# Kernel optimization log

Hardware: AMD Instinct MI355X
Metric: run time of the kernel (lower is better)

The kernel has to match this reference:

```python
import jax, jax.numpy as jnp
import numpy as np

K = 4            # number of modes (init kwarg)
ALPHA = 2000.0   # bandwidth constraint
TAU = 0.0        # dual ascent step (0 -> exact reconstruction slack)
N_ITERS = 20     # fixed ADMM iterations (orig: tol-based while loop, max 500)


def vmd_batch(x):
    # x: [B, C, T] float32 -> (u: [B, C, K, T], omega: [B, C, K])
    B, C, T = x.shape
    T2 = 2 * T
    half = T2 // 2
    # mirror extension (vmdpy): flip first half | signal | flip second half
    f = jnp.concatenate([x[..., :T // 2][..., ::-1], x, x[..., T // 2:][..., ::-1]], axis=-1)  # [B,C,T2]
    t = jnp.arange(1, T2 + 1, dtype=jnp.float32) / T2
    freqs = t - 0.5 - 1.0 / T2                       # [T2], centered frequency axis
    freqs_pos = freqs[half:]                          # [T], positive frequencies
    f_hat = jnp.fft.fftshift(jnp.fft.fft(f, axis=-1), axes=-1).astype(jnp.complex64)
    f_hat_plus = f_hat.at[..., :half].set(0.0)        # keep analytic (positive-freq) part
    # init=1: uniform initial center frequencies
    omega = jnp.broadcast_to((0.5 / K) * jnp.arange(K, dtype=jnp.float32), (B, C, K))
    u_hat = jnp.zeros((B, C, K, T2), dtype=jnp.complex64)
    lam = jnp.zeros((B, C, T2), dtype=jnp.complex64)  # dual variable lambda_hat

    def step(carry, _):
        u_hat, omega, lam = carry
        S = jnp.sum(u_hat, axis=2)                    # running sum of all modes [B,C,T2]
        new_u, new_w = [], []
        for k in range(K):                            # Gauss-Seidel sweep over K modes (K small, unrolled)
            S = S - u_hat[:, :, k]                    # sum of all other modes (updated ones included)
            denom = 1.0 + ALPHA * (freqs[None, None, :] - omega[:, :, k:k + 1]) ** 2
            uk = (f_hat_plus - S + lam / 2.0) / denom # Wiener-filter spectral update [B,C,T2]
            S = S + uk
            p = uk.real[..., half:] ** 2 + uk.imag[..., half:] ** 2  # power on positive freqs [B,C,T]
            wk = jnp.sum(freqs_pos * p, axis=-1) / jnp.sum(p, axis=-1)  # center-frequency re-estimate
            new_u.append(uk)
            new_w.append(wk)
        u_hat = jnp.stack(new_u, axis=2)
        omega = jnp.stack(new_w, axis=-1)
        lam = lam + TAU * (S - f_hat_plus)            # dual ascent (tau=0 -> no-op, kept for fidelity)
        return (u_hat, omega, lam), None

    (u_hat, omega, lam), _ = jax.lax.scan(step, (u_hat, omega, lam), None, length=N_ITERS)

    # reconstruct full conjugate-symmetric spectrum
    pos = u_hat[..., half:]                           # [B,C,K,T]
    full = jnp.zeros((B, C, K, T2), dtype=jnp.complex64)
    full = full.at[..., half:].set(pos)
    full = full.at[..., 1:half + 1].set(jnp.conj(pos)[..., ::-1])  # full[half-j] = conj(pos[j])
    full = full.at[..., 0].set(jnp.conj(full[..., -1]))
    u = jnp.real(jnp.fft.ifft(jnp.fft.ifftshift(full, axes=-1), axis=-1))  # [B,C,K,T2]
    u = u[..., T2 // 4: 3 * T2 // 4]                  # de-mirror: center T samples
    return u, omega


def setup_inputs() -> dict:
    key = jax.random.key(0)
    x = jax.random.normal(key, (16, 8192, 4), dtype=jnp.float32)  # [B, T, C]
    return {"x": x}


def reference(x):
    # module forward: permute [B,T,C] -> [B,C,T], run VMD, return u:[B,K,T,C], omega:[B,K]
    u, omega = vmd_batch(jnp.transpose(x, (0, 2, 1)))
    u = jnp.transpose(u, (0, 2, 3, 1))                # [B,K,T,C]
    omega_b = jnp.mean(omega, axis=1)                 # collapse channel dim -> [B,K]
    return (u, omega_b)
```

## Files before the change

kernel.cpp:

```cpp
#include <hip/hip_runtime.h>


#define HALF      8192
#define NH        8192
#define NTHREADS  1024
#define KMODES    4
#define NITERS    20
#define ALPHA_F   2000.0f
#define SQH       0.70710678118654752440f
#define NSPLIT    4
#define SENTINEL  0xFFFFFFFFu

typedef __fp16 half2_t __attribute__((ext_vector_type(2)));
typedef float  v2f     __attribute__((ext_vector_type(2)));

__device__ __forceinline__ unsigned bitrev13(unsigned x) { return __brev(x) >> 19; }
__device__ __forceinline__ int pidx(int i) { return i + (i >> 4); }

__device__ __forceinline__ unsigned pack_h2(float a, float b) {
    half2_t h = __builtin_amdgcn_cvt_pkrtz(a, b);
    return __builtin_bit_cast(unsigned, h);
}
__device__ __forceinline__ v2f unpack_h2(unsigned u) {
    half2_t h = __builtin_bit_cast(half2_t, u);
    v2f r; r.x = (float)h.x; r.y = (float)h.y; return r;
}

template <int CTRL>
__device__ __forceinline__ float dpp_add_step(float v) {
    int r = __builtin_amdgcn_update_dpp(0, __float_as_int(v), CTRL, 0xf, 0xf, true);
    return v + __int_as_float(r);
}
__device__ __forceinline__ float wave64_sum(float v) {
    v = dpp_add_step<0x111>(v);
    v = dpp_add_step<0x112>(v);
    v = dpp_add_step<0x114>(v);
    v = dpp_add_step<0x118>(v);
    v = dpp_add_step<0x142>(v);
    v = dpp_add_step<0x143>(v);
    return v;
}

__device__ __forceinline__ float2 cmul(float2 a, float wr, float wi) {
    return make_float2(a.x * wr - a.y * wi, a.x * wi + a.y * wr);
}
__device__ __forceinline__ float2 cadd(float2 a, float2 b) {
    return make_float2(a.x + b.x, a.y + b.y);
}
__device__ __forceinline__ float2 csub(float2 a, float2 b) {
    return make_float2(a.x - b.x, a.y - b.y);
}

template <bool INV>
__device__ __forceinline__ void fft_pass8(float2* A, int tid, int t) {
    const int   log2Q = 10 - 3 * t;
    const int   Q     = 1 << log2Q;
    const float invL  = (float)(1 << (3 * t)) * (1.0f / 8192.0f);
    const int j    = tid & (Q - 1);
    const int base = ((tid >> log2Q) << (log2Q + 3)) + j;

    float2 x[8];
    #pragma unroll
    for (int m = 0; m < 8; ++m) x[m] = A[pidx(base + m * Q)];

    float rev = (float)j * invL;
    float w1r = __builtin_amdgcn_cosf(rev);
    float w1i = INV ?  __builtin_amdgcn_sinf(rev)
                    : -__builtin_amdgcn_sinf(rev);
    float w2r = w1r * w1r - w1i * w1i, w2i = 2.0f * w1r * w1i;
    float w4r = w2r * w2r - w2i * w2i, w4i = 2.0f * w2r * w2i;
    float wsr, wsi;
    if (INV) { wsr = SQH * (w1r - w1i); wsi = SQH * (w1r + w1i); }
    else     { wsr = SQH * (w1r + w1i); wsi = SQH * (w1i - w1r); }
    float w1tr = INV ? -w1i : w1i,  w1ti = INV ? w1r : -w1r;
    float wstr = INV ? -wsi : wsi,  wsti = INV ? wsr : -wsr;
    float w2tr = INV ? -w2i : w2i,  w2ti = INV ? w2r : -w2r;

    float2 y0 = cadd(x[0], x[4]), y1 = cadd(x[1], x[5]);
    float2 y2 = cadd(x[2], x[6]), y3 = cadd(x[3], x[7]);
    float2 y4 = cmul(csub(x[0], x[4]), w1r, w1i);
    float2 y5 = cmul(csub(x[1], x[5]), wsr, wsi);
    float2 y6 = cmul(csub(x[2], x[6]), w1tr, w1ti);
    float2 y7 = cmul(csub(x[3], x[7]), wstr, wsti);

    float2 z0 = cadd(y0, y2), z2 = cmul(csub(y0, y2), w2r, w2i);
    float2 z1 = cadd(y1, y3), z3 = cmul(csub(y1, y3), w2tr, w2ti);
    float2 z4 = cadd(y4, y6), z6 = cmul(csub(y4, y6), w2r, w2i);
    float2 z5 = cadd(y5, y7), z7 = cmul(csub(y5, y7), w2tr, w2ti);

    A[pidx(base + 0 * Q)] = cadd(z0, z1);
    A[pidx(base + 1 * Q)] = cmul(csub(z0, z1), w4r, w4i);
    A[pidx(base + 2 * Q)] = cadd(z2, z3);
    A[pidx(base + 3 * Q)] = cmul(csub(z2, z3), w4r, w4i);
    A[pidx(base + 4 * Q)] = cadd(z4, z5);
    A[pidx(base + 5 * Q)] = cmul(csub(z4, z5), w4r, w4i);
    A[pidx(base + 6 * Q)] = cadd(z6, z7);
    A[pidx(base + 7 * Q)] = cmul(csub(z6, z7), w4r, w4i);
}

__device__ __forceinline__ void fft_last2(float2* A, int tid) {
    #pragma unroll
    for (int u = 0; u < 4; ++u) {
        int t  = tid + u * NTHREADS;
        int i0 = 2 * t, i1 = 2 * t + 1;
        float2 a = A[pidx(i0)], b = A[pidx(i1)];
        A[pidx(i0)] = make_float2(a.x + b.x, a.y + b.y);
        A[pidx(i1)] = make_float2(a.x - b.x, a.y - b.y);
    }
}

__device__ __forceinline__ int mirror_t(int i) {
    if (i < 4096)       return 4095 - i;
    else if (i < 12288) return i - 4096;
    else                return 20479 - i;
}

__global__ __launch_bounds__(NTHREADS) void vmd_forward_iter(
    const float* __restrict__ x, unsigned* __restrict__ ws_u,
    float* __restrict__ ws_omega, unsigned* __restrict__ ws_part)
{
    __shared__ float2 A[NH + (NH >> 4)];
    const int tid = threadIdx.x;
    const int bid = blockIdx.x;
    const int ch  = bid & 63;
    const int q   = bid >> 6;
    const int b   = ch >> 2, c = ch & 3;
    const float* xb = x + (size_t)b * 8192 * 4 + c;

    for (int m = tid; m < NH; m += NTHREADS) {
        float re = xb[(size_t)mirror_t(2 * m) * 4];
        float im = xb[(size_t)mirror_t(2 * m + 1) * 4];
        A[pidx(m)] = make_float2(re, im);
    }
    __syncthreads();

    for (int t = 0; t < 4; ++t) {
        fft_pass8<false>(A, tid, t);
        __syncthreads();
    }
    fft_last2(A, tid);
    __syncthreads();

    v2f R[2];
    #pragma unroll
    for (int u = 0; u < 2; ++u) {
        int j  = (q << 11) + tid + u * NTHREADS;
        float2 z1 = A[pidx((int)bitrev13((unsigned)j))];
        float2 z2 = A[pidx((int)bitrev13((unsigned)((NH - j) & (NH - 1))))];
        float ex = 0.5f * (z1.x + z2.x);
        float ey = 0.5f * (z1.y - z2.y);
        float dx = 0.5f * (z1.x - z2.x);
        float dy = 0.5f * (z1.y + z2.y);
        float rev = (float)j * (1.0f / 16384.0f);
        float wr = __builtin_amdgcn_cosf(rev);
        float wi = -__builtin_amdgcn_sinf(rev);
        R[u].x = ex + wr * dy + wi * dx;
        R[u].y = ey + wi * dy - wr * dx;
    }
    __syncthreads();

    v2f Up[KMODES][2];
    #pragma unroll
    for (int u = 0; u < 2; ++u)
        #pragma unroll
        for (int k = 0; k < KMODES; ++k) { Up[k][u].x = 0.f; Up[k][u].y = 0.f; }

    const float f0 = (float)((q << 11) + tid) * (1.0f / 16384.0f);
    float omg[KMODES] = {0.0f, 0.125f, 0.25f, 0.375f};

    float* red = (float*)A;
    const int lane = tid & 63, wid = tid >> 6;

    for (int it = 0; it < NITERS; ++it) {
        v2f nd[KMODES];
        #pragma unroll
        for (int k = 0; k < KMODES; ++k) { nd[k].x = 0.f; nd[k].y = 0.f; }
        #pragma unroll
        for (int u = 0; u < 2; ++u) {
            const float fru = f0 + (float)u * 0.0625f;
            v2f fv; fv.x = fru; fv.y = 1.0f;
            #pragma unroll
            for (int k = 0; k < KMODES; ++k) {
                float d   = fru - omg[k];
                float dnm = fmaf(ALPHA_F * d, d, 1.0f);
                float rcp = __builtin_amdgcn_rcpf(dnm);
                v2f uo  = Up[k][u];
                v2f nm  = R[u] + uo;
                v2f un  = nm * rcp;
                R[u]    = nm - un;
                Up[k][u] = un;
                float p = fmaf(un.x, un.x, un.y * un.y);
                nd[k]   = fv * p + nd[k];
            }
        }
        float num[KMODES], den[KMODES];
        #pragma unroll
        for (int m = 0; m < KMODES; ++m) {
            num[m] = wave64_sum(nd[m].x);
            den[m] = wave64_sum(nd[m].y);
        }
        float* redb = red + (it & 1) * 144;
        if (lane == 63) {
            float4* r4 = (float4*)&redb[wid * 8];
            r4[0] = make_float4(num[0], num[1], num[2], num[3]);
            r4[1] = make_float4(den[0], den[1], den[2], den[3]);
        }
        __syncthreads();
        unsigned* pp = ws_part + (((size_t)it * 64 + ch) << 5);
        if (wid == 0) {
            float v = redb[lane] + redb[lane + 64];
            v += __int_as_float(__builtin_amdgcn_ds_swizzle(__float_as_int(v), 0x201F));
            v += __int_as_float(__builtin_amdgcn_ds_swizzle(__float_as_int(v), 0x401F));
            v += __int_as_float(__builtin_amdgcn_ds_bpermute((lane ^ 32) << 2,
                                                             __float_as_int(v)));
            if (lane < 8)
                __hip_atomic_store(pp + (q << 3) + lane, __float_as_uint(v),
                                   __ATOMIC_RELAXED, __HIP_MEMORY_SCOPE_AGENT);
            float t = 0.0f;
            if (lane < 32) {
                unsigned w;
                for (;;) {
                    w = __hip_atomic_load(pp + lane, __ATOMIC_RELAXED,
                                          __HIP_MEMORY_SCOPE_AGENT);
                    if (w != SENTINEL) break;
                    __builtin_amdgcn_s_sleep(1);
                }
                t = __uint_as_float(w);
            }
            t += __int_as_float(__builtin_amdgcn_ds_swizzle(__float_as_int(t), 0x201F));
            t += __int_as_float(__builtin_amdgcn_ds_swizzle(__float_as_int(t), 0x401F));
            if (lane < 8) redb[128 + lane] = t;
        }
        __syncthreads();
        #pragma unroll
        for (int m = 0; m < KMODES; ++m) {
            float nm_ = redb[128 + m];
            float dn_ = redb[128 + m + 4];
            omg[m] = nm_ * __builtin_amdgcn_rcpf(dn_);
        }
    }

    #pragma unroll
    for (int k = 0; k < KMODES; ++k) {
        unsigned* dst = ws_u + (size_t)(ch * KMODES + k) * HALF + (q << 11);
        #pragma unroll
        for (int u = 0; u < 2; ++u)
            dst[tid + u * NTHREADS] = pack_h2(Up[k][u].x, Up[k][u].y);
    }
    if (q == 0 && tid < KMODES) ws_omega[ch * KMODES + tid] = omg[tid];
}

__global__ __launch_bounds__(NTHREADS) void vmd_inverse(
    const unsigned* __restrict__ ws_u, const float* __restrict__ ws_omega,
    float* __restrict__ out)
{
    __shared__ float2 A[NH + (NH >> 4)];
    const int tid = threadIdx.x;
    const int bid = blockIdx.x;
    const int g   = bid & 63;
    const int c   = bid >> 6;
    const int b   = g >> 2, k = g & 3;
    const int ch  = b * 4 + c;
    const unsigned* pos = ws_u + (size_t)(ch * KMODES + k) * HALF;

    if (bid == 0 && tid < 64) {
        int bb = tid >> 2, kk = tid & 3;
        float s = 0.f;
        #pragma unroll
        for (int cc = 0; cc < 4; ++cc) s += ws_omega[(bb * 4 + cc) * 4 + kk];
        out[2097152 + tid] = 0.25f * s;
    }

    for (int j = tid; j < NH; j += NTHREADS) {
        v2f pj = unpack_h2(pos[j]);
        v2f ph = unpack_h2(pos[j ? (HALF - j) : (HALF - 1)]);
        float gjx = pj.x, gjy = (j == 0) ? -pj.y : pj.y;
        float ghx = ph.x, ghy = -ph.y;
        float ex = 0.5f * (gjx + ghx), ey = 0.5f * (gjy + ghy);
        float dx = 0.5f * (gjx - ghx), dy = 0.5f * (gjy - ghy);
        float rev = (float)j * (1.0f / 16384.0f);
        float wr = __builtin_amdgcn_cosf(rev);
        float wi = __builtin_amdgcn_sinf(rev);
        float ox = dx * wr - dy * wi;
        float oy = dx * wi + dy * wr;
        A[pidx(j)] = make_float2(ex - oy, ey + ox);
    }
    __syncthreads();

    for (int t = 0; t < 4; ++t) {
        fft_pass8<true>(A, tid, t);
        __syncthreads();
    }
    fft_last2(A, tid);
    __syncthreads();

    float* outp = out + (size_t)(b * 4 + k) * 8192 * 4 + c;
    for (int m = 2048 + tid; m < 6144; m += NTHREADS) {
        float2 z = A[pidx((int)bitrev13((unsigned)m))];
        int t0 = 2 * m - 4096;
        outp[(size_t)t0 * 4]       = z.x * (1.0f / 8192.0f);
        outp[(size_t)(t0 + 1) * 4] = z.y * (1.0f / 8192.0f);
    }
}

extern "C" void kernel_launch(void* const* d_in, const int* in_sizes, int n_in,
                              void* d_out, int out_size, void* d_ws, size_t ws_size,
                              hipStream_t stream)
{
    (void)in_sizes; (void)n_in; (void)out_size; (void)ws_size;
    const float* x = (const float*)d_in[0];
    float* out = (float*)d_out;

    unsigned* ws_u     = (unsigned*)d_ws;
    float*    ws_omega = (float*)((char*)d_ws + (size_t)64 * 4 * HALF * 4);
    unsigned* ws_part  = (unsigned*)((char*)d_ws + (size_t)64 * 4 * HALF * 4 + 1024);

    hipMemsetAsync(ws_part, 0xFF, (size_t)NITERS * 64 * 32 * 4, stream);
    vmd_forward_iter<<<256, NTHREADS, 0, stream>>>(x, ws_u, ws_omega, ws_part);
    vmd_inverse<<<256, NTHREADS, 0, stream>>>(ws_u, ws_omega, out);
}
```

Measured before the change: 81.75 us.

## Replace block barriers with LDS atomic last-wave reduction and per-wave global polling

```diff
diff --git a/kernel.cpp b/kernel.cpp
--- a/kernel.cpp
+++ b/kernel.cpp
@@ -4,6 +4,7 @@
 #define HALF      8192
 #define NH        8192
 #define NTHREADS  1024
+#define NWAVES    16
 #define KMODES    4
 #define NITERS    20
 #define ALPHA_F   2000.0f
@@ -120,12 +121,17 @@
     float* __restrict__ ws_omega, unsigned* __restrict__ ws_part)
 {
     __shared__ float2 A[NH + (NH >> 4)];
+    __shared__ float  acc[NITERS][8];
+    __shared__ int    cnt[NITERS];
     const int tid = threadIdx.x;
     const int bid = blockIdx.x;
     const int ch  = bid & 63;
     const int q   = bid >> 6;
     const int b   = ch >> 2, c = ch & 3;
     const float* xb = x + (size_t)b * 8192 * 4 + c;
+
+    if (tid < NITERS * 8) ((float*)acc)[tid] = 0.0f;
+    if (tid < NITERS)     cnt[tid] = 0;
 
     for (int m = tid; m < NH; m += NTHREADS) {
         float re = xb[(size_t)mirror_t(2 * m) * 4];
@@ -157,7 +163,6 @@
         R[u].x = ex + wr * dy + wi * dx;
         R[u].y = ey + wi * dy - wr * dx;
     }
-    __syncthreads();
 
     v2f Up[KMODES][2];
     #pragma unroll
@@ -168,8 +173,7 @@
     const float f0 = (float)((q << 11) + tid) * (1.0f / 16384.0f);
     float omg[KMODES] = {0.0f, 0.125f, 0.25f, 0.375f};
 
-    float* red = (float*)A;
-    const int lane = tid & 63, wid = tid >> 6;
+    const int lane = tid & 63;
 
     for (int it = 0; it < NITERS; ++it) {
         v2f nd[KMODES];
@@ -199,43 +203,46 @@
             num[m] = wave64_sum(nd[m].x);
             den[m] = wave64_sum(nd[m].y);
         }
-        float* redb = red + (it & 1) * 144;
+        unsigned* pp = ws_part + (((size_t)it * 64 + ch) << 5);
+        int old = 0;
         if (lane == 63) {
-            float4* r4 = (float4*)&redb[wid * 8];
-            r4[0] = make_float4(num[0], num[1], num[2], num[3]);
-            r4[1] = make_float4(den[0], den[1], den[2], den[3]);
-        }
-        __syncthreads();
-        unsigned* pp = ws_part + (((size_t)it * 64 + ch) << 5);
-        if (wid == 0) {
-            float v = redb[lane] + redb[lane + 64];
-            v += __int_as_float(__builtin_amdgcn_ds_swizzle(__float_as_int(v), 0x201F));
-            v += __int_as_float(__builtin_amdgcn_ds_swizzle(__float_as_int(v), 0x401F));
-            v += __int_as_float(__builtin_amdgcn_ds_bpermute((lane ^ 32) << 2,
-                                                             __float_as_int(v)));
-            if (lane < 8)
-                __hip_atomic_store(pp + (q << 3) + lane, __float_as_uint(v),
+            #pragma unroll
+            for (int m = 0; m < KMODES; ++m) {
+                __hip_atomic_fetch_add(&acc[it][m],     num[m], __ATOMIC_RELAXED,
+                                       __HIP_MEMORY_SCOPE_WORKGROUP);
+                __hip_atomic_fetch_add(&acc[it][m + 4], den[m], __ATOMIC_RELAXED,
+                                       __HIP_MEMORY_SCOPE_WORKGROUP);
+            }
+            asm volatile("s_waitcnt lgkmcnt(0)" ::: "memory");
+            old = __hip_atomic_fetch_add(&cnt[it], 1, __ATOMIC_RELAXED,
+                                         __HIP_MEMORY_SCOPE_WORKGROUP);
+        }
+        int lastw = __builtin_amdgcn_readlane(old, 63);
+        if (lastw == NWAVES - 1) {
+            if (lane < 8) {
+                float bp = __hip_atomic_load(&acc[it][lane], __ATOMIC_RELAXED,
+                                             __HIP_MEMORY_SCOPE_WORKGROUP);
+                __hip_atomic_store(pp + (q << 3) + lane, __float_as_uint(bp),
                                    __ATOMIC_RELAXED, __HIP_MEMORY_SCOPE_AGENT);
-            float t = 0.0f;
-            if (lane < 32) {
-                unsigned w;
-                for (;;) {
-                    w = __hip_atomic_load(pp + lane, __ATOMIC_RELAXED,
-                                          __HIP_MEMORY_SCOPE_AGENT);
-                    if (w != SENTINEL) break;
-                    __builtin_amdgcn_s_sleep(1);
-                }
-                t = __uint_as_float(w);
             }
-            t += __int_as_float(__builtin_amdgcn_ds_swizzle(__float_as_int(t), 0x201F));
-            t += __int_as_float(__builtin_amdgcn_ds_swizzle(__float_as_int(t), 0x401F));
-            if (lane < 8) redb[128 + lane] = t;
-        }
-        __syncthreads();
+        }
+        float t = 0.0f;
+        if (lane < 32) {
+            unsigned w;
+            for (;;) {
+                w = __hip_atomic_load(pp + lane, __ATOMIC_RELAXED,
+                                      __HIP_MEMORY_SCOPE_AGENT);
+                if (w != SENTINEL) break;
+                __builtin_amdgcn_s_sleep(1);
+            }
+            t = __uint_as_float(w);
+        }
+        t += __int_as_float(__builtin_amdgcn_ds_swizzle(__float_as_int(t), 0x201F));
+        t += __int_as_float(__builtin_amdgcn_ds_swizzle(__float_as_int(t), 0x401F));
         #pragma unroll
         for (int m = 0; m < KMODES; ++m) {
-            float nm_ = redb[128 + m];
-            float dn_ = redb[128 + m + 4];
+            float nm_ = __int_as_float(__builtin_amdgcn_readlane(__float_as_int(t), m));
+            float dn_ = __int_as_float(__builtin_amdgcn_readlane(__float_as_int(t), m + 4));
             omg[m] = nm_ * __builtin_amdgcn_rcpf(dn_);
         }
     }
```

New measurement: 102.9 us. 25.9% more time.
